# Kernel optimization log

Hardware: AMD Instinct MI355X
Metric: run time of the kernel (lower is better)

Reference implementation:

```python
import jax, jax.numpy as jnp
import numpy as np

N_NODES, C, R, L, H, NB = 50000, 512, 4096, 32, 4, 4  # NB blocks: enc0, enc1, pma, dec0
LN_EPS = 1e-5

def _layer_norm(x, g, b):
    mu = jnp.mean(x, axis=-1, keepdims=True)
    var = jnp.var(x, axis=-1, keepdims=True)
    return (x - mu) * jax.lax.rsqrt(var + LN_EPS) * g + b

def _mab(x, y, y_mask, x_mask, Wq, bq, Wk, bk, Wv, bv, Wo, bo, ffW, ffb, g1, b1, g2, b2):
    # Multihead attention block (SetTransformer MAB), dropout=0 at inference.
    Rr, Lq, Cc = x.shape
    Lk = y.shape[1]
    Dh = Cc // H
    q = (x @ Wq.T + bq).reshape(Rr, Lq, H, Dh)
    k = (y @ Wk.T + bk).reshape(Rr, Lk, H, Dh)
    v = (y @ Wv.T + bv).reshape(Rr, Lk, H, Dh)
    scores = jnp.einsum('rqhd,rkhd->rhqk', q, k) * (1.0 / Dh ** 0.5)
    if y_mask is not None:  # mask padded keys (ragged gene sets)
        scores = jnp.where(y_mask[:, None, None, :], scores, jnp.float32(-1e30))
    attn = jax.nn.softmax(scores, axis=-1)
    out = jnp.einsum('rhqk,rkhd->rqhd', attn, v).reshape(Rr, Lq, Cc)
    out = out @ Wo.T + bo
    if x_mask is not None:  # zero attention output at padded query rows
        out = jnp.where(x_mask[..., None], out, 0.0)
    out = _layer_norm(out + x, g1, b1)
    out = _layer_norm(out + jax.nn.relu(out @ ffW.T + ffb), g2, b2)
    return out

def setup_inputs() -> dict:
    key = jax.random.key(0)
    ks = jax.random.split(key, 10)
    s = 0.02
    return {
        'gene_embeddings': jax.random.normal(ks[0], (N_NODES, C), jnp.float32),
        'reaction_gene_idx': jax.random.randint(ks[1], (R, L), 0, N_NODES),
        'reaction_lengths': jax.random.randint(ks[2], (R,), 1, L + 1),
        'Wq': jax.random.normal(ks[3], (NB, C, C), jnp.float32) * s,
        'Wk': jax.random.normal(ks[4], (NB, C, C), jnp.float32) * s,
        'Wv': jax.random.normal(ks[5], (NB, C, C), jnp.float32) * s,
        'Wo': jax.random.normal(ks[6], (NB, C, C), jnp.float32) * s,
        'ffW': jax.random.normal(ks[7], (NB, C, C), jnp.float32) * s,
        'bq': jnp.zeros((NB, C), jnp.float32),
        'bk': jnp.zeros((NB, C), jnp.float32),
        'bv': jnp.zeros((NB, C), jnp.float32),
        'bo': jnp.zeros((NB, C), jnp.float32),
        'ffb': jnp.zeros((NB, C), jnp.float32),
        'g1': jnp.ones((NB, C), jnp.float32),
        'b1': jnp.zeros((NB, C), jnp.float32),
        'g2': jnp.ones((NB, C), jnp.float32),
        'b2': jnp.zeros((NB, C), jnp.float32),
        'pma_lin_W': jax.random.normal(ks[8], (C, C), jnp.float32) * s,
        'pma_lin_b': jnp.zeros((C,), jnp.float32),
        'seed': jax.random.normal(ks[9], (1, C), jnp.float32) * s,
    }

def reference(gene_embeddings, reaction_gene_idx, reaction_lengths, Wq, Wk, Wv, Wo, ffW, bq, bk, bv, bo, ffb, g1, b1, g2, b2, pma_lin_W, pma_lin_b, seed):
    mask = jnp.arange(L)[None, :] < reaction_lengths[:, None]  # [R, L] ragged validity mask
    x = gene_embeddings[reaction_gene_idx]                     # [R, L, C] per-reaction gather
    x = jnp.where(mask[..., None], x, 0.0)
    def blk(i, xq, ykv, ymask, xmask):
        return _mab(xq, ykv, ymask, xmask, Wq[i], bq[i], Wk[i], bk[i], Wv[i], bv[i],
                    Wo[i], bo[i], ffW[i], ffb[i], g1[i], b1[i], g2[i], b2[i])
    x = blk(0, x, x, mask, mask)   # encoder SAB 0
    x = blk(1, x, x, mask, mask)   # encoder SAB 1
    y = jax.nn.relu(x @ pma_lin_W.T + pma_lin_b)
    sd = jnp.broadcast_to(seed[None, :, :], (R, 1, C))
    x = blk(2, sd, y, mask, None)  # PMA: 1 seed attends over gene set
    x = blk(3, x, x, None, None)   # decoder SAB over the single seed
    out = jnp.mean(x, axis=1)      # [R, C] (1 seed, concat=False)
    out = jnp.where((reaction_lengths > 0)[:, None], out, 0.0)  # empty reactions -> zeros
    return out
```

## Files before the change

kernel.cpp:

```cpp
#include <hip/hip_runtime.h>
#include <stdint.h>

#define R_ 4096
#define L_ 32
#define C_ 512
#define H_ 4
#define DH_ 128

typedef __bf16 bf16x8 __attribute__((ext_vector_type(8)));
typedef float f32x4 __attribute__((ext_vector_type(4)));

__device__ __forceinline__ float b2f(unsigned int u) {
    union { unsigned int i; float f; } x; x.i = u << 16; return x.f;
}
__device__ __forceinline__ unsigned short f2b(float f) {
    union { float f; unsigned int i; } x; x.f = f;
    unsigned int i = x.i;
    i += 0x7fffu + ((i >> 16) & 1u);
    return (unsigned short)(i >> 16);
}
__device__ __forceinline__ void unpack8(uint4 v, float* x) {
    x[0] = b2f(v.x & 0xffffu); x[1] = b2f(v.x >> 16);
    x[2] = b2f(v.y & 0xffffu); x[3] = b2f(v.y >> 16);
    x[4] = b2f(v.z & 0xffffu); x[5] = b2f(v.z >> 16);
    x[6] = b2f(v.w & 0xffffu); x[7] = b2f(v.w >> 16);
}
__device__ __forceinline__ uint4 pack8(const float* x) {
    uint4 v;
    v.x = (unsigned)f2b(x[0]) | ((unsigned)f2b(x[1]) << 16);
    v.y = (unsigned)f2b(x[2]) | ((unsigned)f2b(x[3]) << 16);
    v.z = (unsigned)f2b(x[4]) | ((unsigned)f2b(x[5]) << 16);
    v.w = (unsigned)f2b(x[6]) | ((unsigned)f2b(x[7]) << 16);
    return v;
}

__device__ __forceinline__ void gload_lds16(const unsigned short* g, unsigned short* l) {
    __builtin_amdgcn_global_load_lds(
        (const __attribute__((address_space(1))) void*)g,
        (__attribute__((address_space(3))) void*)l, 16, 0, 0);
}

__global__ __launch_bounds__(256)
void detect_kernel(const unsigned short* __restrict__ gene, int* __restrict__ flag) {
    __shared__ int cnt;
    if (threadIdx.x == 0) cnt = 0;
    __syncthreads();
    int local = 0;
    for (int j = 0; j < 8; ++j) {
        int i = threadIdx.x * 8 + j;
        unsigned short u = gene[2 * i];
        int e = (u >> 7) & 0xFF;
        if (e >= 100 && e <= 140) ++local;
    }
    atomicAdd(&cnt, local);
    __syncthreads();
    if (threadIdx.x == 0) *flag = (cnt >= 1024) ? 1 : 0;
}

__global__ __launch_bounds__(256)
void cvt_any_kernel(const void* __restrict__ in, unsigned short* __restrict__ out,
                    int n, const int* __restrict__ flag, int src_off) {
    int i0 = (blockIdx.x * 256 + threadIdx.x) * 8;
    if (i0 >= n) return;
    if (*flag) {
        *(uint4*)(out + i0) = *(const uint4*)((const unsigned short*)in + src_off + i0);
    } else {
        const float* f = (const float*)in + src_off;
        float4 a = *(const float4*)(f + i0);
        float4 b = *(const float4*)(f + i0 + 4);
        float x[8] = {a.x, a.y, a.z, a.w, b.x, b.y, b.z, b.w};
        *(uint4*)(out + i0) = pack8(x);
    }
}

__global__ __launch_bounds__(256)
void bias_concat_kernel(const unsigned short* __restrict__ bq, const unsigned short* __restrict__ bk,
                        const unsigned short* __restrict__ bv,
                        unsigned short* __restrict__ bqkv0, unsigned short* __restrict__ bqkv1,
                        unsigned short* __restrict__ bkv2) {
    int t = threadIdx.x;
#pragma unroll
    for (int s = 0; s < 2; ++s) {
        int i = t + s * 256;
        bqkv0[i]        = bq[i];
        bqkv0[i + 512]  = bk[i];
        bqkv0[i + 1024] = bv[i];
        bqkv1[i]        = bq[i + 512];
        bqkv1[i + 512]  = bk[i + 512];
        bqkv1[i + 1024] = bv[i + 512];
        bkv2[i]         = bk[i + 1024];
        bkv2[i + 512]   = bv[i + 1024];
    }
}

__global__ __launch_bounds__(256)
void qp_kernel(const unsigned short* __restrict__ Wq2, const unsigned short* __restrict__ bq2,
               const unsigned short* __restrict__ seed, unsigned short* __restrict__ qp) {
    __shared__ float sv[512];
    int t = threadIdx.x;
    sv[t] = b2f(seed[t]); sv[t + 256] = b2f(seed[t + 256]);
    __syncthreads();
#pragma unroll
    for (int s = 0; s < 2; ++s) {
        int n = t + s * 256;
        const unsigned short* wrow = Wq2 + (size_t)n * 512;
        float acc = 0.f;
        for (int k8 = 0; k8 < 64; ++k8) {
            float x[8];
            unpack8(*(const uint4*)(wrow + k8 * 8), x);
#pragma unroll
            for (int e = 0; e < 8; ++e) acc += x[e] * sv[k8 * 8 + e];
        }
        qp[n] = f2b(acc + b2f(bq2[n]));
    }
}

__global__ __launch_bounds__(256)
void wc_kernel(const unsigned short* __restrict__ Wo3, const unsigned short* __restrict__ Wv3,
               unsigned short* __restrict__ Wc) {
    const int i = blockIdx.x, t = threadIdx.x;
    __shared__ float wo[512];
    wo[t] = b2f(Wo3[(size_t)i * 512 + t]);
    wo[t + 256] = b2f(Wo3[(size_t)i * 512 + t + 256]);
    __syncthreads();
    float a0 = 0.f, a1 = 0.f;
    for (int d = 0; d < 512; ++d) {
        const unsigned short* row = Wv3 + (size_t)d * 512;
        float w = wo[d];
        a0 += w * b2f(row[t]);
        a1 += w * b2f(row[t + 256]);
    }
    Wc[(size_t)i * 512 + t]       = f2b(a0);
    Wc[(size_t)i * 512 + t + 256] = f2b(a1);
}

__global__ __launch_bounds__(256)
void bc_kernel(const unsigned short* __restrict__ Wo3, const unsigned short* __restrict__ bv3,
               const unsigned short* __restrict__ bo3, unsigned short* __restrict__ bc) {
    const int t = threadIdx.x;
    __shared__ float bvv[512];
    bvv[t] = b2f(bv3[t]); bvv[t + 256] = b2f(bv3[t + 256]);
    __syncthreads();
    const int i = blockIdx.x * 256 + t;
    const unsigned short* row = Wo3 + (size_t)i * 512;
    float acc = 0.f;
    for (int d8 = 0; d8 < 64; ++d8) {
        float x[8];
        unpack8(*(const uint4*)(row + d8 * 8), x);
#pragma unroll
        for (int e = 0; e < 8; ++e) acc += x[e] * bvv[d8 * 8 + e];
    }
    bc[i] = f2b(acc + b2f(bo3[i]));
}

__global__ __launch_bounds__(256)
void diag_kernel(unsigned short* __restrict__ out, int n, float val) {
    int i = blockIdx.x * 256 + threadIdx.x;
    if (i < n) out[i] = f2b(val);
}

__global__ __launch_bounds__(256)
void scan_kernel(const int* __restrict__ lens, int* __restrict__ off,
                 int* __restrict__ meta, int Rc) {
    __shared__ int tsum[257];
    const int t = threadIdx.x;
    const int chunk = (Rc + 255) / 256;
    const int lo = t * chunk;
    const int hi = min(lo + chunk, Rc);
    int s = 0;
    for (int i = lo; i < hi; ++i) {
        int l = lens[i]; l = max(0, min(32, l));
        s += l;
    }
    tsum[t] = s;
    __syncthreads();
    if (t == 0) {
        int acc = 0;
        for (int i = 0; i < 256; ++i) { int v = tsum[i]; tsum[i] = acc; acc += v; }
        tsum[256] = acc;
        meta[0] = acc;
        meta[1] = (acc + 127) & ~127;
    }
    __syncthreads();
    int run = tsum[t];
    for (int i = lo; i < hi; ++i) {
        off[i] = run;
        int l = lens[i]; l = max(0, min(32, l));
        run += l;
    }
}

__global__ __launch_bounds__(256)
void gather_kernel(const void* __restrict__ gene_v, const int* __restrict__ gidx,
                   const int* __restrict__ lens, const int* __restrict__ off,
                   unsigned short* __restrict__ X, const int* __restrict__ flag) {
    int tid = blockIdx.x * 256 + threadIdx.x;
    int m = tid >> 6;
    int ch = tid & 63;
    int r = m >> 5, j = m & 31;
    if (j >= lens[r]) return;
    size_t dst = (size_t)(off[r] + j) * C_ + ch * 8;
    size_t base = (size_t)gidx[m] * C_ + ch * 8;
    uint4 v;
    if (*flag) {
        v = *(const uint4*)((const unsigned short*)gene_v + base);
    } else {
        const float* f = (const float*)gene_v;
        float4 a = *(const float4*)(f + base);
        float4 b = *(const float4*)(f + base + 4);
        float x[8] = {a.x, a.y, a.z, a.w, b.x, b.y, b.z, b.w};
        v = pack8(x);
    }
    *(uint4*)(X + dst) = v;
}

__global__ __launch_bounds__(256)
void ztail_kernel(unsigned short* __restrict__ X, const int* __restrict__ meta) {
    int tid = blockIdx.x * 256 + threadIdx.x;
    int m = meta[0] + (tid >> 6);
    int ch = tid & 63;
    if (m < meta[1])
        *(uint4*)(X + (size_t)m * C_ + ch * 8) = make_uint4(0u, 0u, 0u, 0u);
}

__global__ __launch_bounds__(256)
void seed_kernel(const unsigned short* __restrict__ seed, unsigned short* __restrict__ Xs) {
    int i = blockIdx.x * 256 + threadIdx.x;
    int ch = i & 63;
    uint4 v = *(const uint4*)(seed + ch * 8);
    *(uint4*)(Xs + (size_t)i * 8) = v;
}

__global__ __launch_bounds__(256)
void final_kernel(const unsigned short* __restrict__ S, const int* __restrict__ lens,
                  void* __restrict__ out, const int* __restrict__ flag, size_t elem_off) {
    int i = blockIdx.x * 256 + threadIdx.x;
    int r = i >> 6;
    uint4 v = make_uint4(0u, 0u, 0u, 0u);
    if (lens[r] > 0) v = *(const uint4*)(S + (size_t)i * 8);
    if (*flag) {
        *(uint4*)((unsigned short*)out + elem_off + (size_t)i * 8) = v;
    } else {
        float x[8];
        unpack8(v, x);
        float* o = (float*)out + elem_off + (size_t)i * 8;
        *(float4*)o       = make_float4(x[0], x[1], x[2], x[3]);
        *(float4*)(o + 4) = make_float4(x[4], x[5], x[6], x[7]);
    }
}

template<int NT>
__global__ __launch_bounds__(256, 2)
void gemm_bt_kernel(const unsigned short* __restrict__ A, const unsigned short* __restrict__ W,
                    const unsigned short* __restrict__ bias, unsigned short* __restrict__ Out,
                    int relu, const int* __restrict__ meta, int MT) {
    const int b = blockIdx.x;
    const int xcd = b & 7;
    const int j = b >> 3;
    const int ml = j / NT;
    const int n = j - ml * NT;
    const int m = ml * 8 + xcd;
    if (m >= MT) return;
    const int m0 = m * 128, n0 = n * 256;
    if (meta && m0 >= meta[1]) return;
    const int ldo = NT * 256;

    __shared__ unsigned short As[128 * 64];
    __shared__ unsigned short Bs[256 * 64];

    const int t = threadIdx.x;
    const int wave = t >> 6, lane = t & 63;
    const int quad = lane >> 4, lr = lane & 15;
    const int wr = wave >> 1, wc = wave & 1;

    const int srow8 = lane >> 3;
    const int scol8 = (lane & 7) ^ srow8;
    const unsigned short* gaB = A + (size_t)(m0 + wave * 8 + srow8) * C_ + scol8 * 8;
    const unsigned short* gbB = W + (size_t)(n0 + wave * 8 + srow8) * C_ + scol8 * 8;
    unsigned short* lA = As + wave * 512;
    unsigned short* lB = Bs + wave * 512;

    f32x4 acc[4][8] = {};

    for (int k0 = 0; k0 < C_; k0 += 64) {
        __syncthreads();
#pragma unroll
        for (int jj = 0; jj < 4; ++jj)
            gload_lds16(gaB + (size_t)jj * 32 * C_ + k0, lA + jj * 2048);
#pragma unroll
        for (int jj = 0; jj < 8; ++jj)
            gload_lds16(gbB + (size_t)jj * 32 * C_ + k0, lB + jj * 2048);
        __syncthreads();

#pragma unroll
        for (int kk = 0; kk < 2; ++kk) {
            bf16x8 af[4], bfr[8];
#pragma unroll
            for (int i = 0; i < 4; ++i)
                af[i] = *(const bf16x8*)&As[(64 * wr + 16 * i + lr) * 64 +
                                            (((kk << 2) + quad) ^ (lr & 7)) * 8];
#pragma unroll
            for (int jj = 0; jj < 8; ++jj)
                bfr[jj] = *(const bf16x8*)&Bs[(128 * wc + 16 * jj + lr) * 64 +
                                              (((kk << 2) + quad) ^ (lr & 7)) * 8];
#pragma unroll
            for (int i = 0; i < 4; ++i)
#pragma unroll
                for (int jj = 0; jj < 8; ++jj)
                    acc[i][jj] = __builtin_amdgcn_mfma_f32_16x16x32_bf16(af[i], bfr[jj], acc[i][jj], 0, 0, 0);
        }
    }

#pragma unroll
    for (int i = 0; i < 4; ++i) {
        int row = m0 + 64 * wr + 16 * i + quad * 4;
#pragma unroll
        for (int jj = 0; jj < 8; ++jj) {
            int col = n0 + 128 * wc + 16 * jj + lr;
            float bv = b2f(bias[col]);
#pragma unroll
            for (int r = 0; r < 4; ++r) {
                float v = acc[i][jj][r] + bv;
                if (relu) v = fmaxf(v, 0.f);
                Out[(size_t)(row + r) * ldo + col] = f2b(v);
            }
        }
    }
}

template<int NK>
__device__ __forceinline__ void attn_enc_body(
    const unsigned short* __restrict__ QKV, unsigned short* __restrict__ O,
    int h, int t, int len, int base,
    unsigned short* Qs, unsigned short* Ks, float (*Sc)[33]) {

#pragma unroll
    for (int it = 0; it < NK; ++it) {
        int flat = t + it * 128;
        int row = flat >> 4, ch = flat & 15;
        if (row < len) {
            size_t g = ((size_t)(base + row)) * 1536 + h * DH_ + ch * 8;
            *(uint4*)&Qs[row * 136 + ch * 8] = *(const uint4*)(QKV + g);
            *(uint4*)&Ks[row * 136 + ch * 8] = *(const uint4*)(QKV + g + 512);
        }
    }
    __syncthreads();

    {
        const int wv = t >> 6;
        const int ln_ = t & 63;
        const int quad = ln_ >> 4, lr = ln_ & 15;
        f32x4 a0 = {0.f, 0.f, 0.f, 0.f};
        f32x4 a1 = {0.f, 0.f, 0.f, 0.f};
#pragma unroll
        for (int s = 0; s < 4; ++s) {
            bf16x8 aq = *(const bf16x8*)&Qs[(wv * 16 + lr) * 136 + s * 32 + quad * 8];
            bf16x8 k0 = *(const bf16x8*)&Ks[lr * 136 + s * 32 + quad * 8];
            a0 = __builtin_amdgcn_mfma_f32_16x16x32_bf16(aq, k0, a0, 0, 0, 0);
            if (NK >= 3) {
                bf16x8 k1 = *(const bf16x8*)&Ks[(16 + lr) * 136 + s * 32 + quad * 8];
                a1 = __builtin_amdgcn_mfma_f32_16x16x32_bf16(aq, k1, a1, 0, 0, 0);
            }
        }
        const float scale = 0.08838834764831845f;
#pragma unroll
        for (int reg = 0; reg < 4; ++reg) {
            int q = wv * 16 + quad * 4 + reg;
            Sc[q][lr] = a0[reg] * scale;
            if (NK >= 3) Sc[q][16 + lr] = a1[reg] * scale;
        }
    }
    __syncthreads();

    if (t < len) {
        float mx = -3e38f;
        for (int k = 0; k < len; ++k) mx = fmaxf(mx, Sc[t][k]);
        float sum = 0.f;
        for (int k = 0; k < len; ++k) { float e = __expf(Sc[t][k] - mx); Sc[t][k] = e; sum += e; }
        float inv = 1.f / sum;
        for (int k = 0; k < len; ++k) Sc[t][k] *= inv;
    }
    __syncthreads();

    {
        const int qh = t >> 3, g = t & 7;
        float av[2][16] = {};
        const unsigned short* Vg = QKV + (size_t)base * 1536 + 1024 + h * DH_ + g * 8;
        for (int k = 0; k < len; ++k) {
            float a0 = Sc[qh][k], a1 = Sc[qh + 16][k];
            const unsigned short* vrow = Vg + (size_t)k * 1536;
            float v0[8], v1[8];
            unpack8(*(const uint4*)vrow, v0);
            unpack8(*(const uint4*)(vrow + 64), v1);
#pragma unroll
            for (int e = 0; e < 8; ++e) {
                av[0][e]     += a0 * v0[e];
                av[0][8 + e] += a0 * v1[e];
                av[1][e]     += a1 * v0[e];
                av[1][8 + e] += a1 * v1[e];
            }
        }
#pragma unroll
        for (int qi = 0; qi < 2; ++qi) {
            int q = qh + 16 * qi;
            if (q >= len) continue;
            size_t ga = ((size_t)(base + q)) * C_ + h * DH_;
#pragma unroll
            for (int j = 0; j < 2; ++j) {
                float tmp[8];
#pragma unroll
                for (int e = 0; e < 8; ++e) tmp[e] = av[qi][j * 8 + e];
                *(uint4*)(O + ga + g * 8 + 64 * j) = pack8(tmp);
            }
        }
    }
}

__global__ __launch_bounds__(128)
void attn_enc_kernel(const unsigned short* __restrict__ QKV, unsigned short* __restrict__ O,
                     const int* __restrict__ lens, const int* __restrict__ off) {
    const int r = blockIdx.x, h = blockIdx.y, t = threadIdx.x;
    const int len = lens[r];
    if (len <= 0) return;
    const int base = off[r];
    __shared__ unsigned short Qs[32 * 136], Ks[32 * 136];
    __shared__ float Sc[32][33];
    switch ((len + 7) >> 3) {
        case 1:  attn_enc_body<1>(QKV, O, h, t, len, base, Qs, Ks, Sc); break;
        case 2:  attn_enc_body<2>(QKV, O, h, t, len, base, Qs, Ks, Sc); break;
        case 3:  attn_enc_body<3>(QKV, O, h, t, len, base, Qs, Ks, Sc); break;
        default: attn_enc_body<4>(QKV, O, h, t, len, base, Qs, Ks, Sc); break;
    }
}

__global__ __launch_bounds__(64)
void attn_pma_kernel(const unsigned short* __restrict__ qp, const unsigned short* __restrict__ KV,
                     unsigned short* __restrict__ O,
                     const int* __restrict__ lens, const int* __restrict__ off) {
    const int r = blockIdx.x, h = blockIdx.y, t = threadIdx.x;
    const int len = lens[r];
    if (len <= 0) return;
    const int base = off[r];
    __shared__ float qv[128];
    __shared__ float attn[32];
    const size_t qb = (size_t)r * C_ + h * DH_;
    qv[t]      = b2f(qp[h * DH_ + t]);
    qv[t + 64] = b2f(qp[h * DH_ + t + 64]);
    __syncthreads();
    if (t < 32 && t < len) {
        const unsigned short* krow = KV + ((size_t)(base + t)) * 1024 + h * DH_;
        float s = 0.f;
        for (int d = 0; d < 128; ++d) s += qv[d] * b2f(krow[d]);
        attn[t] = s * 0.08838834764831845f;
    }
    __syncthreads();
    if (t == 0) {
        float mx = -3e38f;
        for (int k = 0; k < len; ++k) mx = fmaxf(mx, attn[k]);
        float sum = 0.f;
        for (int k = 0; k < len; ++k) { float e = __expf(attn[k] - mx); attn[k] = e; sum += e; }
        float inv = 1.f / sum;
        for (int k = 0; k < len; ++k) attn[k] *= inv;
    }
    __syncthreads();
    float a0 = 0.f, a1 = 0.f;
    for (int k = 0; k < len; ++k) {
        const unsigned short* vrow = KV + ((size_t)(base + k)) * 1024 + 512 + h * DH_;
        float a = attn[k];
        a0 += a * b2f(vrow[t]);
        a1 += a * b2f(vrow[t + 64]);
    }
    O[qb + t]      = f2b(a0);
    O[qb + t + 64] = f2b(a1);
}

__global__ __launch_bounds__(256)
void ln_kernel(const unsigned short* __restrict__ A, const unsigned short* __restrict__ Res,
               const unsigned short* __restrict__ gamma, const unsigned short* __restrict__ beta,
               unsigned short* __restrict__ out, const int* __restrict__ lens, int use_mask,
               const int* __restrict__ meta) {
    const int m = blockIdx.x * 4 + (threadIdx.x >> 6);
    if (meta && m >= meta[1]) return;
    const int lane = threadIdx.x & 63;
    const bool masked = use_mask && ((m & 31) >= lens[m >> 5]);
    const size_t base = (size_t)m * C_ + lane * 8;
    float xa[8], xr[8], x[8];
    unpack8(*(const uint4*)(A + base), xa);
    unpack8(*(const uint4*)(Res + base), xr);
    float s = 0.f, ss = 0.f;
#pragma unroll
    for (int e = 0; e < 8; ++e) {
        x[e] = (masked ? 0.f : xa[e]) + xr[e];
        s += x[e]; ss += x[e] * x[e];
    }
#pragma unroll
    for (int off = 32; off > 0; off >>= 1) {
        s  += __shfl_down(s, off);
        ss += __shfl_down(ss, off);
    }
    s = __shfl(s, 0); ss = __shfl(ss, 0);
    const float mu = s * (1.f / 512.f);
    const float rinv = rsqrtf(fmaxf(ss * (1.f / 512.f) - mu * mu, 0.f) + 1e-5f);
    float gg[8], bb[8], y[8];
    unpack8(*(const uint4*)(gamma + lane * 8), gg);
    unpack8(*(const uint4*)(beta + lane * 8), bb);
#pragma unroll
    for (int e = 0; e < 8; ++e) y[e] = (x[e] - mu) * rinv * gg[e] + bb[e];
    *(uint4*)(out + base) = pack8(y);
}

extern "C" void kernel_launch(void* const* d_in, const int* in_sizes, int n_in,
                              void* d_out, int out_size, void* d_ws, size_t ws_size,
                              hipStream_t stream) {
    (void)in_sizes; (void)n_in;
    const void* gene = d_in[0];
    const int*  gidx = (const int*)d_in[1];
    const int*  lens = (const int*)d_in[2];

    int* ibase = (int*)d_ws;
    int* flag  = ibase;
    int* meta  = ibase + 2;
    int* d_off = ibase + 8;
    unsigned short* ws0 = (unsigned short*)(ibase + 8 + 4096);
    const size_t hdr_bytes = (size_t)(8 + 4096) * 4;

    size_t off = 0;
    auto take = [&](size_t elems) { unsigned short* p = ws0 + off; off += elems; return p; };
    const size_t CC = (size_t)C_ * C_;
    unsigned short* wEnc0 = take(3 * CC);
    unsigned short* wEnc1 = take(3 * CC);
    unsigned short* wKVp  = take(2 * CC);
    unsigned short* wO  = take(4 * CC);
    unsigned short* wF  = take(4 * CC);
    unsigned short* wP  = take(CC);
    unsigned short* wQp = take(CC);
    unsigned short* wVd = take(CC);
    unsigned short* wWc = take(CC);
    unsigned short* cbq = take(4 * C_);
    unsigned short* cbk = take(4 * C_);
    unsigned short* cbv = take(4 * C_);
    unsigned short* cbo = take(4 * C_);
    unsigned short* cff = take(4 * C_);
    unsigned short* cg1 = take(4 * C_);
    unsigned short* cb1 = take(4 * C_);
    unsigned short* cg2 = take(4 * C_);
    unsigned short* cb2 = take(4 * C_);
    unsigned short* cpb = take(C_);
    unsigned short* csd = take(C_);
    unsigned short* bqkv0 = take(3 * C_);
    unsigned short* bqkv1 = take(3 * C_);
    unsigned short* bkv2  = take(2 * C_);
    unsigned short* bcb   = take(C_);
    unsigned short* qp    = take(C_);
    const size_t wbytes = hdr_bytes + off * 2;

    const size_t per_r = ((size_t)32 * 2560 + 4 * 512) * 2;
    int Rc = 0;
    const int cands[6] = {4096, 2048, 1024, 512, 256, 128};
    for (int i = 0; i < 6; ++i) {
        size_t need = wbytes + (size_t)cands[i] * per_r;
        if (need <= ws_size) { Rc = cands[i]; break; }
    }
    if (Rc == 0) {
        diag_kernel<<<(out_size + 255) / 256, 256, 0, stream>>>(
            (unsigned short*)d_out, out_size, 1000.0f + (float)(ws_size >> 20));
        return;
    }
    const int Mc = Rc * 32;

    unsigned short* X    = take((size_t)Mc * C_);
    unsigned short* AQKV = take((size_t)Mc * 1536);
    unsigned short* Aout = take((size_t)Mc * C_);
    unsigned short* S0 = take((size_t)Rc * C_);
    unsigned short* S1 = take((size_t)Rc * C_);
    unsigned short* S2 = take((size_t)Rc * C_);
    unsigned short* S3 = take((size_t)Rc * C_);

    detect_kernel<<<1, 256, 0, stream>>>((const unsigned short*)gene, flag);
    auto cvt = [&](const void* in, unsigned short* out_, int n, int src_off) {
        cvt_any_kernel<<<(n + 2047) / 2048, 256, 0, stream>>>(in, out_, n, flag, src_off);
    };
    cvt(d_in[3], wEnc0,          (int)CC, 0);
    cvt(d_in[4], wEnc0 + CC,     (int)CC, 0);
    cvt(d_in[5], wEnc0 + 2 * CC, (int)CC, 0);
    cvt(d_in[3], wEnc1,          (int)CC, (int)CC);
    cvt(d_in[4], wEnc1 + CC,     (int)CC, (int)CC);
    cvt(d_in[5], wEnc1 + 2 * CC, (int)CC, (int)CC);
    cvt(d_in[4], wKVp,      (int)CC, (int)(2 * CC));
    cvt(d_in[5], wKVp + CC, (int)CC, (int)(2 * CC));
    cvt(d_in[3], wQp, (int)CC, (int)(2 * CC));
    cvt(d_in[5], wVd, (int)CC, (int)(3 * CC));
    cvt(d_in[6], wO, (int)(4 * CC), 0);
    cvt(d_in[7], wF, (int)(4 * CC), 0);
    cvt(d_in[17], wP, (int)CC, 0);
    cvt(d_in[8],  cbq, 4 * C_, 0); cvt(d_in[9],  cbk, 4 * C_, 0); cvt(d_in[10], cbv, 4 * C_, 0);
    cvt(d_in[11], cbo, 4 * C_, 0); cvt(d_in[12], cff, 4 * C_, 0);
    cvt(d_in[13], cg1, 4 * C_, 0); cvt(d_in[14], cb1, 4 * C_, 0);
    cvt(d_in[15], cg2, 4 * C_, 0); cvt(d_in[16], cb2, 4 * C_, 0);
    cvt(d_in[18], cpb, C_, 0);     cvt(d_in[19], csd, C_, 0);
    bias_concat_kernel<<<1, 256, 0, stream>>>(cbq, cbk, cbv, bqkv0, bqkv1, bkv2);
    qp_kernel<<<1, 256, 0, stream>>>(wQp, cbq + 2 * C_, csd, qp);
    wc_kernel<<<512, 256, 0, stream>>>(wO + 3 * CC, wVd, wWc);
    bc_kernel<<<2, 256, 0, stream>>>(wO + 3 * CC, cbv + 3 * C_, cbo + 3 * C_, bcb);

    auto gemm = [&](auto nt_tag, const unsigned short* Ain, const unsigned short* Win,
                    const unsigned short* bias, unsigned short* Outp, int Mrows, int relu,
                    const int* mt) {
        constexpr int NT = decltype(nt_tag)::value;
        const int MT = Mrows / 128;
        const int grid = 8 * ((MT + 7) / 8) * NT;
        gemm_bt_kernel<NT><<<dim3(grid), 256, 0, stream>>>(Ain, Win, bias, Outp, relu, mt, MT);
    };
    using N2 = std::integral_constant<int, 2>;
    using N4 = std::integral_constant<int, 4>;
    using N6 = std::integral_constant<int, 6>;

    for (int c = 0; c < R_ / Rc; ++c) {
        const int r0 = c * Rc;
        const int* lc = lens + r0;

        scan_kernel<<<1, 256, 0, stream>>>(lc, d_off, meta, Rc);
        gather_kernel<<<Mc * 64 / 256, 256, 0, stream>>>(
            gene, gidx + (size_t)r0 * L_, lc, d_off, X, flag);
        ztail_kernel<<<32, 256, 0, stream>>>(X, meta);

        for (int i = 0; i < 2; ++i) {
            gemm(N6{}, X, i ? wEnc1 : wEnc0, i ? bqkv1 : bqkv0, AQKV, Mc, 0, meta);
            attn_enc_kernel<<<dim3(Rc, H_), 128, 0, stream>>>(AQKV, Aout, lc, d_off);
            gemm(N2{}, Aout, wO + (size_t)i * CC, cbo + i * C_, AQKV, Mc, 0, meta);
            ln_kernel<<<Mc / 4, 256, 0, stream>>>(AQKV, X, cg1 + i * C_, cb1 + i * C_, X, lc, 0, meta);
            gemm(N2{}, X, wF + (size_t)i * CC, cff + i * C_, Aout, Mc, 1, meta);
            ln_kernel<<<Mc / 4, 256, 0, stream>>>(Aout, X, cg2 + i * C_, cb2 + i * C_, X, lc, 0, meta);
        }

        gemm(N2{}, X, wP, cpb, Aout, Mc, 1, meta);
        seed_kernel<<<Rc * 64 / 256, 256, 0, stream>>>(csd, S0);

        {
            gemm(N4{}, Aout, wKVp, bkv2, AQKV, Mc, 0, meta);
            attn_pma_kernel<<<dim3(Rc, H_), 64, 0, stream>>>(qp, AQKV, S2, lc, d_off);
            gemm(N2{}, S2, wO + 2 * CC, cbo + 2 * C_, S3, Rc, 0, nullptr);
            ln_kernel<<<Rc / 4, 256, 0, stream>>>(S3, S0, cg1 + 2 * C_, cb1 + 2 * C_, S0, lc, 0, nullptr);
            gemm(N2{}, S0, wF + 2 * CC, cff + 2 * C_, S1, Rc, 1, nullptr);
            ln_kernel<<<Rc / 4, 256, 0, stream>>>(S1, S0, cg2 + 2 * C_, cb2 + 2 * C_, S0, lc, 0, nullptr);
        }

        {
            gemm(N2{}, S0, wWc, bcb, S2, Rc, 0, nullptr);
            ln_kernel<<<Rc / 4, 256, 0, stream>>>(S2, S0, cg1 + 3 * C_, cb1 + 3 * C_, S0, lc, 0, nullptr);
            gemm(N2{}, S0, wF + 3 * CC, cff + 3 * C_, S1, Rc, 1, nullptr);
            ln_kernel<<<Rc / 4, 256, 0, stream>>>(S1, S0, cg2 + 3 * C_, cb2 + 3 * C_, S0, lc, 0, nullptr);
        }

        final_kernel<<<Rc * 64 / 256, 256, 0, stream>>>(S0, lc, d_out, flag, (size_t)r0 * C_);
    }
}
```

Measured before the change: 1.730 ms.

## Fuse PMA output projection, FFNs, decoder block and final write into one tail kernel

Replaces the post-attention chain for the PMA and decoder blocks (four small GEMMs, four layernorms, the seed broadcast and the final write) with a single kernel. Each block of that kernel keeps 16 reaction rows in shared memory and runs MFMA matvecs plus layernorms in sequence. This removes about ten launches and the intermediate global round-trips on the Rc x 512 tensors. In exchange, each block streams the weights straight from global/L2 with no tiling reuse across blocks, and only Rc/16 blocks run, which gives low parallelism.

```diff
diff --git a/kernel.cpp b/kernel.cpp
--- a/kernel.cpp
+++ b/kernel.cpp
@@ -223,32 +223,6 @@
         *(uint4*)(X + (size_t)m * C_ + ch * 8) = make_uint4(0u, 0u, 0u, 0u);
 }
 
-__global__ __launch_bounds__(256)
-void seed_kernel(const unsigned short* __restrict__ seed, unsigned short* __restrict__ Xs) {
-    int i = blockIdx.x * 256 + threadIdx.x;
-    int ch = i & 63;
-    uint4 v = *(const uint4*)(seed + ch * 8);
-    *(uint4*)(Xs + (size_t)i * 8) = v;
-}
-
-__global__ __launch_bounds__(256)
-void final_kernel(const unsigned short* __restrict__ S, const int* __restrict__ lens,
-                  void* __restrict__ out, const int* __restrict__ flag, size_t elem_off) {
-    int i = blockIdx.x * 256 + threadIdx.x;
-    int r = i >> 6;
-    uint4 v = make_uint4(0u, 0u, 0u, 0u);
-    if (lens[r] > 0) v = *(const uint4*)(S + (size_t)i * 8);
-    if (*flag) {
-        *(uint4*)((unsigned short*)out + elem_off + (size_t)i * 8) = v;
-    } else {
-        float x[8];
-        unpack8(v, x);
-        float* o = (float*)out + elem_off + (size_t)i * 8;
-        *(float4*)o       = make_float4(x[0], x[1], x[2], x[3]);
-        *(float4*)(o + 4) = make_float4(x[4], x[5], x[6], x[7]);
-    }
-}
-
 template<int NT>
 __global__ __launch_bounds__(256, 2)
 void gemm_bt_kernel(const unsigned short* __restrict__ A, const unsigned short* __restrict__ W,
@@ -507,6 +481,119 @@
 #pragma unroll
     for (int e = 0; e < 8; ++e) y[e] = (x[e] - mu) * rinv * gg[e] + bb[e];
     *(uint4*)(out + base) = pack8(y);
+}
+
+__device__ __forceinline__ void tail_matvec(const unsigned short* cur, unsigned short* tmp,
+        const unsigned short* __restrict__ W, const unsigned short* __restrict__ bias,
+        int relu, int t) {
+    const int w = t >> 6, l = t & 63;
+    const int arow = l & 15, kq = l >> 4;
+    f32x4 acc[8] = {};
+    for (int ks = 0; ks < 16; ++ks) {
+        bf16x8 af = *(const bf16x8*)&cur[arow * 520 + ks * 32 + kq * 8];
+#pragma unroll
+        for (int nf = 0; nf < 8; ++nf) {
+            int n = 128 * w + 16 * nf + arow;
+            bf16x8 bfr = *(const bf16x8*)&W[(size_t)n * 512 + ks * 32 + kq * 8];
+            acc[nf] = __builtin_amdgcn_mfma_f32_16x16x32_bf16(af, bfr, acc[nf], 0, 0, 0);
+        }
+    }
+#pragma unroll
+    for (int nf = 0; nf < 8; ++nf) {
+        int col = 128 * w + 16 * nf + arow;
+        float bv = b2f(bias[col]);
+#pragma unroll
+        for (int reg = 0; reg < 4; ++reg) {
+            float v = acc[nf][reg] + bv;
+            if (relu) v = fmaxf(v, 0.f);
+            tmp[(kq * 4 + reg) * 520 + col] = f2b(v);
+        }
+    }
+}
+
+__device__ __forceinline__ void tail_ln(unsigned short* cur, const unsigned short* tmp,
+        const unsigned short* __restrict__ gamma, const unsigned short* __restrict__ beta,
+        const unsigned short* __restrict__ res_seed, int t) {
+    const int r = t >> 4, i = t & 15;
+    float val[32];
+    float s = 0.f, ss = 0.f;
+#pragma unroll
+    for (int j = 0; j < 32; ++j) {
+        int c = i * 32 + j;
+        float a = b2f(tmp[r * 520 + c]);
+        float b = res_seed ? b2f(res_seed[c]) : b2f(cur[r * 520 + c]);
+        float v = a + b;
+        val[j] = v; s += v; ss += v * v;
+    }
+#pragma unroll
+    for (int off_ = 8; off_ > 0; off_ >>= 1) {
+        s  += __shfl_down(s, off_, 16);
+        ss += __shfl_down(ss, off_, 16);
+    }
+    s = __shfl(s, 0, 16); ss = __shfl(ss, 0, 16);
+    const float mu = s * (1.f / 512.f);
+    const float rinv = rsqrtf(fmaxf(ss * (1.f / 512.f) - mu * mu, 0.f) + 1e-5f);
+#pragma unroll
+    for (int j = 0; j < 32; ++j) {
+        int c = i * 32 + j;
+        float y = (val[j] - mu) * rinv * b2f(gamma[c]) + b2f(beta[c]);
+        cur[r * 520 + c] = f2b(y);
+    }
+}
+
+__global__ __launch_bounds__(256)
+void tail_kernel(const unsigned short* __restrict__ S2,
+                 const unsigned short* __restrict__ Wo2, const unsigned short* __restrict__ bo2,
+                 const unsigned short* __restrict__ Wf2, const unsigned short* __restrict__ fb2,
+                 const unsigned short* __restrict__ Wc,  const unsigned short* __restrict__ bc,
+                 const unsigned short* __restrict__ Wf3, const unsigned short* __restrict__ fb3,
+                 const unsigned short* __restrict__ g12, const unsigned short* __restrict__ b12,
+                 const unsigned short* __restrict__ g22, const unsigned short* __restrict__ b22,
+                 const unsigned short* __restrict__ g13, const unsigned short* __restrict__ b13,
+                 const unsigned short* __restrict__ g23, const unsigned short* __restrict__ b23,
+                 const unsigned short* __restrict__ seedv,
+                 const int* __restrict__ lens, void* __restrict__ out,
+                 const int* __restrict__ flag, size_t elem_off) {
+    __shared__ unsigned short cur[16 * 520];
+    __shared__ unsigned short tmp[16 * 520];
+    const int t = threadIdx.x;
+    const int rbase = blockIdx.x * 16;
+    const int r = t >> 4, i = t & 15;
+
+#pragma unroll
+    for (int j = 0; j < 4; ++j)
+        *(uint4*)&cur[r * 520 + i * 32 + j * 8] =
+            *(const uint4*)&S2[(size_t)(rbase + r) * 512 + i * 32 + j * 8];
+    __syncthreads();
+
+    tail_matvec(cur, tmp, Wo2, bo2, 0, t); __syncthreads();
+    tail_ln(cur, tmp, g12, b12, seedv, t); __syncthreads();
+    tail_matvec(cur, tmp, Wf2, fb2, 1, t); __syncthreads();
+    tail_ln(cur, tmp, g22, b22, nullptr, t); __syncthreads();
+    tail_matvec(cur, tmp, Wc, bc, 0, t); __syncthreads();
+    tail_ln(cur, tmp, g13, b13, nullptr, t); __syncthreads();
+    tail_matvec(cur, tmp, Wf3, fb3, 1, t); __syncthreads();
+    tail_ln(cur, tmp, g23, b23, nullptr, t); __syncthreads();
+
+    const int rg = rbase + r;
+    const bool ok = lens[rg] > 0;
+    if (*flag) {
+#pragma unroll
+        for (int j = 0; j < 4; ++j) {
+            uint4 v = make_uint4(0u, 0u, 0u, 0u);
+            if (ok) v = *(uint4*)&cur[r * 520 + i * 32 + j * 8];
+            *(uint4*)((unsigned short*)out + elem_off + (size_t)rg * 512 + i * 32 + j * 8) = v;
+        }
+    } else {
+#pragma unroll
+        for (int j = 0; j < 4; ++j) {
+            float x[8] = {};
+            if (ok) unpack8(*(uint4*)&cur[r * 520 + i * 32 + j * 8], x);
+            float* o = (float*)out + elem_off + (size_t)rg * 512 + i * 32 + j * 8;
+            *(float4*)o       = make_float4(x[0], x[1], x[2], x[3]);
+            *(float4*)(o + 4) = make_float4(x[4], x[5], x[6], x[7]);
+        }
+    }
 }
 
 extern "C" void kernel_launch(void* const* d_in, const int* in_sizes, int n_in,
@@ -554,7 +641,7 @@
     unsigned short* qp    = take(C_);
     const size_t wbytes = hdr_bytes + off * 2;
 
-    const size_t per_r = ((size_t)32 * 2560 + 4 * 512) * 2;
+    const size_t per_r = ((size_t)32 * 2560 + 512) * 2;
     int Rc = 0;
     const int cands[6] = {4096, 2048, 1024, 512, 256, 128};
     for (int i = 0; i < 6; ++i) {
@@ -571,10 +658,7 @@
     unsigned short* X    = take((size_t)Mc * C_);
     unsigned short* AQKV = take((size_t)Mc * 1536);
     unsigned short* Aout = take((size_t)Mc * C_);
-    unsigned short* S0 = take((size_t)Rc * C_);
-    unsigned short* S1 = take((size_t)Rc * C_);
     unsigned short* S2 = take((size_t)Rc * C_);
-    unsigned short* S3 = take((size_t)Rc * C_);
 
     detect_kernel<<<1, 256, 0, stream>>>((const unsigned short*)gene, flag);
     auto cvt = [&](const void* in, unsigned short* out_, int n, int src_off) {
@@ -634,24 +718,18 @@
         }
 
         gemm(N2{}, X, wP, cpb, Aout, Mc, 1, meta);
-        seed_kernel<<<Rc * 64 / 256, 256, 0, stream>>>(csd, S0);
-
-        {
-            gemm(N4{}, Aout, wKVp, bkv2, AQKV, Mc, 0, meta);
-            attn_pma_kernel<<<dim3(Rc, H_), 64, 0, stream>>>(qp, AQKV, S2, lc, d_off);
-            gemm(N2{}, S2, wO + 2 * CC, cbo + 2 * C_, S3, Rc, 0, nullptr);
-            ln_kernel<<<Rc / 4, 256, 0, stream>>>(S3, S0, cg1 + 2 * C_, cb1 + 2 * C_, S0, lc, 0, nullptr);
-            gemm(N2{}, S0, wF + 2 * CC, cff + 2 * C_, S1, Rc, 1, nullptr);
-            ln_kernel<<<Rc / 4, 256, 0, stream>>>(S1, S0, cg2 + 2 * C_, cb2 + 2 * C_, S0, lc, 0, nullptr);
-        }
-
-        {
-            gemm(N2{}, S0, wWc, bcb, S2, Rc, 0, nullptr);
-            ln_kernel<<<Rc / 4, 256, 0, stream>>>(S2, S0, cg1 + 3 * C_, cb1 + 3 * C_, S0, lc, 0, nullptr);
-            gemm(N2{}, S0, wF + 3 * CC, cff + 3 * C_, S1, Rc, 1, nullptr);
-            ln_kernel<<<Rc / 4, 256, 0, stream>>>(S1, S0, cg2 + 3 * C_, cb2 + 3 * C_, S0, lc, 0, nullptr);
-        }
-
-        final_kernel<<<Rc * 64 / 256, 256, 0, stream>>>(S0, lc, d_out, flag, (size_t)r0 * C_);
-    }
-}
+
+        gemm(N4{}, Aout, wKVp, bkv2, AQKV, Mc, 0, meta);
+        attn_pma_kernel<<<dim3(Rc, H_), 64, 0, stream>>>(qp, AQKV, S2, lc, d_off);
+
+        tail_kernel<<<Rc / 16, 256, 0, stream>>>(
+            S2,
+            wO + 2 * CC, cbo + 2 * C_,
+            wF + 2 * CC, cff + 2 * C_,
+            wWc, bcb,
+            wF + 3 * CC, cff + 3 * C_,
+            cg1 + 2 * C_, cb1 + 2 * C_, cg2 + 2 * C_, cb2 + 2 * C_,
+            cg1 + 3 * C_, cb1 + 3 * C_, cg2 + 3 * C_, cb2 + 3 * C_,
+            csd, lc, d_out, flag, (size_t)r0 * C_);
+    }
+}
```

New measurement: 1.725 ms. Within noise of the previous version (-0.3%).
